# Optimization experiments

Measured on AMD Instinct MI355X. Metric: run time of the kernel, lower is better.

The kernel has to match this reference:

```python
import jax, jax.numpy as jnp
import numpy as np

N = 50000   # nodes
E = 800000  # edges per graph
FD = 128    # input feature dim (sc and fc)
H = 128     # hidden_dim
G = 64      # graphs in batch
C = 2       # num_classes


def _sage(x, src, dst, Wl, Wr, b, n):
    # PyG SAGEConv (mean aggr): lin_l(mean_{j->i} x_j) + lin_r(x_i); bias lives in lin_l.
    msum = jax.ops.segment_sum(x[src], dst, num_segments=n)          # [n, F]
    cnt = jax.ops.segment_sum(jnp.ones((src.shape[0],), x.dtype), dst, num_segments=n)
    mean = msum / jnp.maximum(cnt, 1.0)[:, None]
    return mean @ Wl.T + x @ Wr.T + b


def setup_inputs() -> dict:
    key = jax.random.key(0)
    ks = jax.random.split(key, 24)
    s = 0.05
    inp = {
        "sc_x": jax.random.normal(ks[0], (N, FD), jnp.float32),
        "fc_x": jax.random.normal(ks[1], (N, FD), jnp.float32),
        "sc_edge_index": jax.random.randint(ks[2], (2, E), 0, N),
        "fc_edge_index": jax.random.randint(ks[3], (2, E), 0, N),
        "batch": jnp.sort(jax.random.randint(ks[4], (N,), 0, G)),
        # sc convs
        "sc_Wl1": jax.random.normal(ks[5], (H, FD), jnp.float32) * s,
        "sc_Wr1": jax.random.normal(ks[6], (H, FD), jnp.float32) * s,
        "sc_b1": jnp.zeros((H,), jnp.float32),
        "sc_Wl2": jax.random.normal(ks[7], (H, H), jnp.float32) * s,
        "sc_Wr2": jax.random.normal(ks[8], (H, H), jnp.float32) * s,
        "sc_b2": jnp.zeros((H,), jnp.float32),
        # fc convs
        "fc_Wl1": jax.random.normal(ks[9], (H, FD), jnp.float32) * s,
        "fc_Wr1": jax.random.normal(ks[10], (H, FD), jnp.float32) * s,
        "fc_b1": jnp.zeros((H,), jnp.float32),
        "fc_Wl2": jax.random.normal(ks[11], (H, H), jnp.float32) * s,
        "fc_Wr2": jax.random.normal(ks[12], (H, H), jnp.float32) * s,
        "fc_b2": jnp.zeros((H,), jnp.float32),
        # MLP head
        "W1": jax.random.normal(ks[13], (H, 2 * H), jnp.float32) * s,
        "bh1": jnp.zeros((H,), jnp.float32),
        "W2": jax.random.normal(ks[14], (H // 2, H), jnp.float32) * s,
        "bh2": jnp.zeros((H // 2,), jnp.float32),
        "W3": jax.random.normal(ks[15], (C, H // 2), jnp.float32) * s,
        "bh3": jnp.zeros((C,), jnp.float32),
    }
    return inp


def reference(sc_x, fc_x, sc_edge_index, fc_edge_index, batch,
              sc_Wl1, sc_Wr1, sc_b1, sc_Wl2, sc_Wr2, sc_b2,
              fc_Wl1, fc_Wr1, fc_b1, fc_Wl2, fc_Wr2, fc_b2,
              W1, bh1, W2, bh2, W3, bh3):
    # edge_index[0] = source j, edge_index[1] = target i (PyG convention)
    sc_src, sc_dst = sc_edge_index[0], sc_edge_index[1]
    fc_src, fc_dst = fc_edge_index[0], fc_edge_index[1]

    h = jax.nn.relu(_sage(sc_x, sc_src, sc_dst, sc_Wl1, sc_Wr1, sc_b1, N))
    h = jax.nn.relu(_sage(h, sc_src, sc_dst, sc_Wl2, sc_Wr2, sc_b2, N))
    sc_pool = jax.ops.segment_sum(h, batch, num_segments=G)  # global_add_pool -> [G, H]

    g = jax.nn.relu(_sage(fc_x, fc_src, fc_dst, fc_Wl1, fc_Wr1, fc_b1, N))
    g = jax.nn.relu(_sage(g, fc_src, fc_dst, fc_Wl2, fc_Wr2, fc_b2, N))
    fc_pool = jax.ops.segment_sum(g, batch, num_segments=G)  # [G, H]

    x = jnp.concatenate([sc_pool, fc_pool], axis=1)          # [G, 2H]
    # dropout is identity in eval mode
    x = jax.nn.relu(x @ W1.T + bh1)
    x = jax.nn.relu(x @ W2.T + bh2)
    return jax.nn.log_softmax(x @ W3.T + bh3, axis=-1)       # [G, C]
```

## Files before the change

### kernel.cpp

```cpp
#include <hip/hip_runtime.h>
#include <hip/hip_bf16.h>

#define N_NODES 50000
#define E_EDGES 800000
#define G_GRAPHS 64
#define NBUCK 392
#define BCAP 5120

typedef __attribute__((ext_vector_type(8))) short s16x8;
typedef __attribute__((ext_vector_type(4))) float f32x4;

constexpr size_t O_POOL   = 0;
constexpr size_t O_GCUR   = 16384;
constexpr size_t O_BSTART = 16896;
constexpr size_t O_ROW    = 17408;
constexpr size_t O_CNT    = 117408;
constexpr size_t O_ES     = 217408;
constexpr size_t O_WB     = 1817408;
constexpr size_t O_XB     = 1882944;
constexpr size_t O_MEAN   = 5082944;
constexpr size_t O_HB     = 8282944;
constexpr size_t ZERO_BYTES = (16384 + 512) * 4;

__device__ __forceinline__ unsigned short f2bf(float f) {
    __hip_bfloat16 h = __float2bfloat16(f);
    return *reinterpret_cast<unsigned short*>(&h);
}
__device__ __forceinline__ float bflo(unsigned int v) { return __uint_as_float(v << 16); }
__device__ __forceinline__ float bfhi(unsigned int v) { return __uint_as_float(v & 0xffff0000u); }

__global__ void __launch_bounds__(512) bin_pass1(const int* __restrict__ sc_e,
                                                 const int* __restrict__ fc_e,
                                                 int* __restrict__ gcur,
                                                 unsigned int* __restrict__ buf) {
    __shared__ int hcnt[512];
    __shared__ int hexcl[512];
    __shared__ int hcur[512];
    __shared__ int gbase[512];
    __shared__ int wsum[8];
    __shared__ unsigned int stage[4096];

    const int tid = threadIdx.x;
    const int lane = tid & 63;
    const int wid = tid >> 6;
    const int tile0 = blockIdx.x * 4096;

    hcnt[tid] = 0;
    __syncthreads();

    int eb[8];
    unsigned int pk[8];
    #pragma unroll
    for (int j = 0; j < 8; ++j) {
        int ec = tile0 + j * 512 + tid;
        if (ec < 2 * E_EDGES) {
            int set = (ec >= E_EDGES);
            int local = ec - set * E_EDGES;
            const int* ep = set ? fc_e : sc_e;
            int src = ep[local];
            int dst = ep[E_EDGES + local];
            eb[j] = set * 196 + (dst >> 8);
            pk[j] = ((unsigned int)(dst & 255) << 16) | (unsigned int)src;
            atomicAdd(&hcnt[eb[j]], 1);
        } else eb[j] = -1;
    }
    __syncthreads();

    {
        int v = hcnt[tid];
        int incl = v;
        #pragma unroll
        for (int d = 1; d < 64; d <<= 1) {
            int u = __shfl_up(incl, d, 64);
            if (lane >= d) incl += u;
        }
        if (lane == 63) wsum[wid] = incl;
        __syncthreads();
        int pre = 0;
        for (int w = 0; w < wid; ++w) pre += wsum[w];
        int excl = incl - v + pre;
        hexcl[tid] = excl;
        hcur[tid] = excl;
    }
    __syncthreads();

    if (tid < NBUCK) {
        int c = hcnt[tid];
        gbase[tid] = c ? atomicAdd(&gcur[tid], c) : 0;
    }

    #pragma unroll
    for (int j = 0; j < 8; ++j) {
        if (eb[j] >= 0) {
            int pos = atomicAdd(&hcur[eb[j]], 1);
            stage[pos] = pk[j];
        }
    }
    __syncthreads();

    for (int b = wid; b < NBUCK; b += 8) {
        int c = hcnt[b];
        if (!c) continue;
        int s = hexcl[b];
        int g0 = gbase[b];
        for (int i = lane; i < c; i += 64) {
            int gi = g0 + i;
            if (gi < BCAP) buf[(size_t)b * BCAP + gi] = stage[s + i];
        }
    }
}

__global__ void bstart_scan(const int* __restrict__ gcur, int* __restrict__ bstart) {
    __shared__ int wsum[8];
    int t = threadIdx.x;
    int lane = t & 63, wid = t >> 6;
    int v = (t < NBUCK) ? min(gcur[t], BCAP) : 0;
    int incl = v;
    #pragma unroll
    for (int d = 1; d < 64; d <<= 1) {
        int u = __shfl_up(incl, d, 64);
        if (lane >= d) incl += u;
    }
    if (lane == 63) wsum[wid] = incl;
    __syncthreads();
    int pre = 0;
    for (int w = 0; w < wid; ++w) pre += wsum[w];
    if (t < NBUCK) bstart[t] = incl - v + pre;
}

__global__ void __launch_bounds__(256) bin_pass2(const unsigned int* __restrict__ buf,
                                                 const int* __restrict__ gcur,
                                                 const int* __restrict__ bstart,
                                                 int* __restrict__ row,
                                                 int* __restrict__ cnt,
                                                 int* __restrict__ es) {
    __shared__ int cntl[256];
    __shared__ int pexcl[256];
    __shared__ int pcur[256];
    __shared__ int wsum[4];
    __shared__ int stage[BCAP];

    const int b = blockIdx.x;
    const int tid = threadIdx.x;
    const int lane = tid & 63, wid = tid >> 6;
    const int sz = min(gcur[b], BCAP);
    const unsigned int* mybuf = buf + (size_t)b * BCAP;
    const int n0 = (b % 196) * 256;
    const int setbase = (b / 196) * N_NODES;

    cntl[tid] = 0;
    __syncthreads();
    for (int i = tid; i < sz; i += 256)
        atomicAdd(&cntl[mybuf[i] >> 16], 1);
    __syncthreads();
    {
        int v = cntl[tid];
        int incl = v;
        #pragma unroll
        for (int d = 1; d < 64; d <<= 1) {
            int u = __shfl_up(incl, d, 64);
            if (lane >= d) incl += u;
        }
        if (lane == 63) wsum[wid] = incl;
        __syncthreads();
        int pre = 0;
        for (int w = 0; w < wid; ++w) pre += wsum[w];
        int excl = incl - v + pre;
        pexcl[tid] = excl;
        pcur[tid] = excl;
    }
    __syncthreads();
    for (int i = tid; i < sz; i += 256) {
        unsigned int p = mybuf[i];
        int pos = atomicAdd(&pcur[p >> 16], 1);
        stage[pos] = (int)(p & 0xFFFFu);
    }
    __syncthreads();
    const int base = bstart[b];
    for (int i = tid; i < sz; i += 256) es[base + i] = stage[i];
    int node = n0 + tid;
    if (node < N_NODES) {
        cnt[setbase + node] = cntl[tid];
        row[setbase + node] = base + pexcl[tid];
    }
}

__global__ void cvt_w_kernel(const float* w0, const float* w1, const float* w2, const float* w3,
                             const float* w4, const float* w5, const float* w6, const float* w7,
                             unsigned short* __restrict__ wb) {
    const float* W;
    int m = blockIdx.y;
    switch (m) {
        case 0: W = w0; break; case 1: W = w1; break;
        case 2: W = w2; break; case 3: W = w3; break;
        case 4: W = w4; break; case 5: W = w5; break;
        case 6: W = w6; break; default: W = w7; break;
    }
    int i = blockIdx.x * 256 + threadIdx.x;
    wb[(size_t)m * 16384 + i] = f2bf(W[i]);
}

__global__ void cvt_x_kernel(const float* __restrict__ src, unsigned short* __restrict__ dst) {
    int i = blockIdx.x * 256 + threadIdx.x;
    if (i >= (N_NODES * 128) / 8) return;
    const float4* s = reinterpret_cast<const float4*>(src) + (size_t)i * 2;
    float4 a = s[0], b = s[1];
    union { s16x8 v; unsigned short u[8]; } p;
    p.u[0] = f2bf(a.x); p.u[1] = f2bf(a.y); p.u[2] = f2bf(a.z); p.u[3] = f2bf(a.w);
    p.u[4] = f2bf(b.x); p.u[5] = f2bf(b.y); p.u[6] = f2bf(b.z); p.u[7] = f2bf(b.w);
    reinterpret_cast<s16x8*>(dst)[i] = p.v;
}

__global__ void __launch_bounds__(256) agg_kernel(const unsigned short* __restrict__ x,
                                                  const int* __restrict__ row,
                                                  const int* __restrict__ cnt,
                                                  const int* __restrict__ es,
                                                  unsigned short* __restrict__ mean,
                                                  int nodebase) {
    int wave = (blockIdx.x * 256 + threadIdx.x) >> 6;
    int lane = threadIdx.x & 63;
    if (wave >= N_NODES) return;
    int gi = nodebase + wave;
    int start = row[gi];
    int deg = cnt[gi];
    float ax = 0.f, ay = 0.f;
    for (int c = 0; c < deg; c += 64) {
        int m = min(64, deg - c);
        int eid = (lane < m) ? es[start + c + lane] : 0;
        int j = 0;
        for (; j + 4 <= m; j += 4) {
            int s0 = __shfl(eid, j,     64);
            int s1 = __shfl(eid, j + 1, 64);
            int s2 = __shfl(eid, j + 2, 64);
            int s3 = __shfl(eid, j + 3, 64);
            unsigned int v0 = *reinterpret_cast<const unsigned int*>(x + (size_t)s0 * 128 + lane * 2);
            unsigned int v1 = *reinterpret_cast<const unsigned int*>(x + (size_t)s1 * 128 + lane * 2);
            unsigned int v2 = *reinterpret_cast<const unsigned int*>(x + (size_t)s2 * 128 + lane * 2);
            unsigned int v3 = *reinterpret_cast<const unsigned int*>(x + (size_t)s3 * 128 + lane * 2);
            ax += bflo(v0) + bflo(v1) + bflo(v2) + bflo(v3);
            ay += bfhi(v0) + bfhi(v1) + bfhi(v2) + bfhi(v3);
        }
        for (; j < m; ++j) {
            int s = __shfl(eid, j, 64);
            unsigned int v = *reinterpret_cast<const unsigned int*>(x + (size_t)s * 128 + lane * 2);
            ax += bflo(v); ay += bfhi(v);
        }
    }
    float inv = 1.0f / fmaxf((float)deg, 1.0f);
    unsigned int r = (unsigned int)f2bf(ax * inv) | ((unsigned int)f2bf(ay * inv) << 16);
    *reinterpret_cast<unsigned int*>(mean + (size_t)wave * 128 + lane * 2) = r;
}

__global__ void __launch_bounds__(256) gemm_mfma(const unsigned short* __restrict__ Am,
                                                 const unsigned short* __restrict__ Ax,
                                                 const unsigned short* __restrict__ Bl,
                                                 const unsigned short* __restrict__ Br,
                                                 const float* __restrict__ bias,
                                                 unsigned short* __restrict__ outH,
                                                 float* __restrict__ pool,
                                                 const int* __restrict__ batch,
                                                 int poolBase) {
    __shared__ s16x8 lds_a[2][256];
    __shared__ s16x8 lds_b[2][512];

    const int tid = threadIdx.x;
    const int lane = tid & 63;
    const int w = tid >> 6;
    const int node0 = blockIdx.x * 64;

    const int wr = w >> 1;
    const int wc = w & 1;
    const int fr = lane & 15;
    const int fg = lane >> 4;

    f32x4 acc[2][4];
    #pragma unroll
    for (int mf = 0; mf < 2; ++mf)
        #pragma unroll
        for (int nf = 0; nf < 4; ++nf) acc[mf][nf] = (f32x4){0.f, 0.f, 0.f, 0.f};

    const int sa_row = tid >> 2, sa_slot = tid & 3;
    const int sa_g = sa_slot ^ ((sa_row >> 1) & 3);
    const size_t a_off = (size_t)min(node0 + sa_row, N_NODES - 1) * 128 + sa_g * 8;
    const int sb_row0 = tid >> 2;
    const size_t b_off0 = (size_t)sb_row0 * 128 + (sa_slot ^ ((sb_row0 >> 1) & 3)) * 8;
    const int sb_row1 = 64 + (tid >> 2);
    const size_t b_off1 = (size_t)sb_row1 * 128 + (sa_slot ^ ((sb_row1 >> 1) & 3)) * 8;

    const int arow0 = wr * 32 + fr;
    const int arow1 = arow0 + 16;
    const int aidx0 = arow0 * 4 + (fg ^ ((arow0 >> 1) & 3));
    const int aidx1 = arow1 * 4 + (fg ^ ((arow1 >> 1) & 3));
    int bidx[4];
    #pragma unroll
    for (int nf = 0; nf < 4; ++nf) {
        int br = wc * 64 + nf * 16 + fr;
        bidx[nf] = br * 4 + (fg ^ ((br >> 1) & 3));
    }

    #define LOAD_A(kc) (*reinterpret_cast<const s16x8*>(((kc) < 4 ? Am : Ax) + (((kc) & 3) * 32) + a_off))
    #define LOAD_B0(kc) (*reinterpret_cast<const s16x8*>(((kc) < 4 ? Bl : Br) + (((kc) & 3) * 32) + b_off0))
    #define LOAD_B1(kc) (*reinterpret_cast<const s16x8*>(((kc) < 4 ? Bl : Br) + (((kc) & 3) * 32) + b_off1))

    {
        s16x8 ra = LOAD_A(0), rb0 = LOAD_B0(0), rb1 = LOAD_B1(0);
        lds_a[0][tid] = ra; lds_b[0][tid] = rb0; lds_b[0][256 + tid] = rb1;
    }
    __syncthreads();

    #pragma unroll
    for (int kc = 0; kc < 8; ++kc) {
        const int cur = kc & 1;
        s16x8 ra, rb0, rb1;
        if (kc < 7) { ra = LOAD_A(kc + 1); rb0 = LOAD_B0(kc + 1); rb1 = LOAD_B1(kc + 1); }
        s16x8 a0 = lds_a[cur][aidx0];
        s16x8 a1 = lds_a[cur][aidx1];
        #pragma unroll
        for (int nf = 0; nf < 4; ++nf) {
            s16x8 bv = lds_b[cur][bidx[nf]];
            acc[0][nf] = __builtin_amdgcn_mfma_f32_16x16x32_bf16(a0, bv, acc[0][nf], 0, 0, 0);
            acc[1][nf] = __builtin_amdgcn_mfma_f32_16x16x32_bf16(a1, bv, acc[1][nf], 0, 0, 0);
        }
        if (kc < 7) { lds_a[cur ^ 1][tid] = ra; lds_b[cur ^ 1][tid] = rb0; lds_b[cur ^ 1][256 + tid] = rb1; }
        __syncthreads();
    }
    #undef LOAD_A
    #undef LOAD_B0
    #undef LOAD_B1

    if (outH) {
        #pragma unroll
        for (int mf = 0; mf < 2; ++mf)
            #pragma unroll
            for (int nf = 0; nf < 4; ++nf) {
                int col = wc * 64 + nf * 16 + fr;
                float bv = bias[col];
                #pragma unroll
                for (int r = 0; r < 4; ++r) {
                    int node = node0 + wr * 32 + mf * 16 + fg * 4 + r;
                    if (node < N_NODES)
                        outH[(size_t)node * 128 + col] = f2bf(fmaxf(acc[mf][nf][r] + bv, 0.f));
                }
            }
    } else {
        int gids[2][4];
        #pragma unroll
        for (int mf = 0; mf < 2; ++mf)
            #pragma unroll
            for (int r = 0; r < 4; ++r) {
                int node = node0 + wr * 32 + mf * 16 + fg * 4 + r;
                gids[mf][r] = (node < N_NODES) ? batch[node] : -1;
            }
        #pragma unroll
        for (int nf = 0; nf < 4; ++nf) {
            int col = wc * 64 + nf * 16 + fr;
            float bv = bias[col];
            float* pbase = &pool[poolBase + col];
            int curg = -1; float s = 0.f;
            #pragma unroll
            for (int mf = 0; mf < 2; ++mf)
                #pragma unroll
                for (int r = 0; r < 4; ++r) {
                    int g = gids[mf][r];
                    if (g < 0) continue;
                    float v = fmaxf(acc[mf][nf][r] + bv, 0.f);
                    if (g != curg) {
                        if (curg >= 0) atomicAdd(pbase + (size_t)curg * 256, s);
                        curg = g; s = v;
                    } else s += v;
                }
            if (curg >= 0) atomicAdd(pbase + (size_t)curg * 256, s);
        }
    }
}

__global__ void __launch_bounds__(128) head_kernel(const float* __restrict__ pool,
                                                   const float* __restrict__ W1, const float* __restrict__ bh1,
                                                   const float* __restrict__ W2, const float* __restrict__ bh2,
                                                   const float* __restrict__ W3, const float* __restrict__ bh3,
                                                   float* __restrict__ out) {
    __shared__ float xg[256];
    __shared__ float h1[128];
    __shared__ float h2[64];
    __shared__ float lg[2];
    int g = blockIdx.x, t = threadIdx.x;
    xg[t] = pool[(size_t)g * 256 + t];
    xg[t + 128] = pool[(size_t)g * 256 + 128 + t];
    __syncthreads();
    float s = bh1[t];
    for (int k = 0; k < 256; ++k) s += W1[t * 256 + k] * xg[k];
    h1[t] = fmaxf(s, 0.f);
    __syncthreads();
    if (t < 64) {
        float s2 = bh2[t];
        for (int k = 0; k < 128; ++k) s2 += W2[t * 128 + k] * h1[k];
        h2[t] = fmaxf(s2, 0.f);
    }
    __syncthreads();
    if (t < 2) {
        float s3 = bh3[t];
        for (int k = 0; k < 64; ++k) s3 += W3[t * 64 + k] * h2[k];
        lg[t] = s3;
    }
    __syncthreads();
    if (t == 0) {
        float m = fmaxf(lg[0], lg[1]);
        float lse = m + logf(expf(lg[0] - m) + expf(lg[1] - m));
        out[g * 2 + 0] = lg[0] - lse;
        out[g * 2 + 1] = lg[1] - lse;
    }
}

extern "C" void kernel_launch(void* const* d_in, const int* in_sizes, int n_in,
                              void* d_out, int out_size, void* d_ws, size_t ws_size,
                              hipStream_t stream) {
    const float* sc_x = (const float*)d_in[0];
    const float* fc_x = (const float*)d_in[1];
    const int* sc_e   = (const int*)d_in[2];
    const int* fc_e   = (const int*)d_in[3];
    const int* batch  = (const int*)d_in[4];
    const float* sc_Wl1 = (const float*)d_in[5];
    const float* sc_Wr1 = (const float*)d_in[6];
    const float* sc_b1  = (const float*)d_in[7];
    const float* sc_Wl2 = (const float*)d_in[8];
    const float* sc_Wr2 = (const float*)d_in[9];
    const float* sc_b2  = (const float*)d_in[10];
    const float* fc_Wl1 = (const float*)d_in[11];
    const float* fc_Wr1 = (const float*)d_in[12];
    const float* fc_b1  = (const float*)d_in[13];
    const float* fc_Wl2 = (const float*)d_in[14];
    const float* fc_Wr2 = (const float*)d_in[15];
    const float* fc_b2  = (const float*)d_in[16];
    const float* W1  = (const float*)d_in[17];
    const float* bh1 = (const float*)d_in[18];
    const float* W2  = (const float*)d_in[19];
    const float* bh2 = (const float*)d_in[20];
    const float* W3  = (const float*)d_in[21];
    const float* bh3 = (const float*)d_in[22];

    int* iw = (int*)d_ws;
    float* fw = (float*)d_ws;
    float* pool = fw + O_POOL;
    int* gcur   = iw + O_GCUR;
    int* bstart = iw + O_BSTART;
    int* row    = iw + O_ROW;
    int* cnt    = iw + O_CNT;
    int* es     = iw + O_ES;
    unsigned short* WB    = (unsigned short*)(iw + O_WB);
    unsigned short* xb    = (unsigned short*)(iw + O_XB);
    unsigned short* meanb = (unsigned short*)(iw + O_MEAN);
    unsigned short* hb    = (unsigned short*)(iw + O_HB);
    unsigned int* buf = (unsigned int*)(iw + O_MEAN);

    hipMemsetAsync(d_ws, 0, ZERO_BYTES, stream);

    bin_pass1<<<(2 * E_EDGES + 4095) / 4096, 512, 0, stream>>>(sc_e, fc_e, gcur, buf);
    bstart_scan<<<1, 512, 0, stream>>>(gcur, bstart);
    bin_pass2<<<NBUCK, 256, 0, stream>>>(buf, gcur, bstart, row, cnt, es);

    cvt_w_kernel<<<dim3(64, 8), 256, 0, stream>>>(sc_Wl1, sc_Wr1, sc_Wl2, sc_Wr2,
                                                  fc_Wl1, fc_Wr1, fc_Wl2, fc_Wr2, WB);

    const int AGB = (N_NODES + 3) / 4;
    const int CVB = ((N_NODES * 128) / 8 + 255) / 256;
    const int GGB = (N_NODES + 63) / 64;

    cvt_x_kernel<<<CVB, 256, 0, stream>>>(sc_x, xb);
    agg_kernel<<<AGB, 256, 0, stream>>>(xb, row, cnt, es, meanb, 0);
    gemm_mfma<<<GGB, 256, 0, stream>>>(meanb, xb, WB + 0 * 16384, WB + 1 * 16384, sc_b1,
                                       hb, nullptr, nullptr, 0);
    agg_kernel<<<AGB, 256, 0, stream>>>(hb, row, cnt, es, meanb, 0);
    gemm_mfma<<<GGB, 256, 0, stream>>>(meanb, hb, WB + 2 * 16384, WB + 3 * 16384, sc_b2,
                                       nullptr, pool, batch, 0);
    cvt_x_kernel<<<CVB, 256, 0, stream>>>(fc_x, xb);
    agg_kernel<<<AGB, 256, 0, stream>>>(xb, row, cnt, es, meanb, N_NODES);
    gemm_mfma<<<GGB, 256, 0, stream>>>(meanb, xb, WB + 4 * 16384, WB + 5 * 16384, fc_b1,
                                       hb, nullptr, nullptr, 0);
    agg_kernel<<<AGB, 256, 0, stream>>>(hb, row, cnt, es, meanb, N_NODES);
    gemm_mfma<<<GGB, 256, 0, stream>>>(meanb, hb, WB + 6 * 16384, WB + 7 * 16384, fc_b2,
                                       nullptr, pool, batch, 128);

    head_kernel<<<G_GRAPHS, 128, 0, stream>>>(pool, W1, bh1, W2, bh2, W3, bh3, (float*)d_out);
}
```

Before: 390.8 us.

## Batch sc and fc branches into shared launches and use quarter-wave 16-byte gathers

Handles the sc and fc graphs in the same kernel launches: one conversion covers both feature sets, and the aggregation and GEMM kernels use a doubled grid, with workspace buffers resized to hold both sets. The aggregation now assigns 16 lanes per node and loads 16 bytes per lane, so a wave processes four nodes in parallel instead of issuing 4-byte loads for one node. This cuts launch count and raises memory-level parallelism and grid fill. In exchange it doubles intermediate buffer footprint, and low-degree nodes may leave quarter-waves idle.

```diff
diff --git a/kernel.cpp b/kernel.cpp
--- a/kernel.cpp
+++ b/kernel.cpp
@@ -6,6 +6,7 @@
 #define G_GRAPHS 64
 #define NBUCK 392
 #define BCAP 5120
+#define NF ((size_t)N_NODES * 128)
 
 typedef __attribute__((ext_vector_type(8))) short s16x8;
 typedef __attribute__((ext_vector_type(4))) float f32x4;
@@ -18,8 +19,8 @@
 constexpr size_t O_ES     = 217408;
 constexpr size_t O_WB     = 1817408;
 constexpr size_t O_XB     = 1882944;
-constexpr size_t O_MEAN   = 5082944;
-constexpr size_t O_HB     = 8282944;
+constexpr size_t O_MEAN   = 8282944;
+constexpr size_t O_HB     = 14682944;
 constexpr size_t ZERO_BYTES = (16384 + 512) * 4;
 
 __device__ __forceinline__ unsigned short f2bf(float f) {
@@ -200,10 +201,14 @@
     wb[(size_t)m * 16384 + i] = f2bf(W[i]);
 }
 
-__global__ void cvt_x_kernel(const float* __restrict__ src, unsigned short* __restrict__ dst) {
+__global__ void cvt_x_kernel(const float* __restrict__ sc_x, const float* __restrict__ fc_x,
+                             unsigned short* __restrict__ dst) {
     int i = blockIdx.x * 256 + threadIdx.x;
-    if (i >= (N_NODES * 128) / 8) return;
-    const float4* s = reinterpret_cast<const float4*>(src) + (size_t)i * 2;
+    if (i >= 2 * (N_NODES * 128) / 8) return;
+    int set = (i >= (N_NODES * 128) / 8);
+    int local = i - set * (N_NODES * 128) / 8;
+    const float* src = set ? fc_x : sc_x;
+    const float4* s = reinterpret_cast<const float4*>(src) + (size_t)local * 2;
     float4 a = s[0], b = s[1];
     union { s16x8 v; unsigned short u[8]; } p;
     p.u[0] = f2bf(a.x); p.u[1] = f2bf(a.y); p.u[2] = f2bf(a.z); p.u[3] = f2bf(a.w);
@@ -215,58 +220,82 @@
                                                   const int* __restrict__ row,
                                                   const int* __restrict__ cnt,
                                                   const int* __restrict__ es,
-                                                  unsigned short* __restrict__ mean,
-                                                  int nodebase) {
+                                                  unsigned short* __restrict__ mean) {
     int wave = (blockIdx.x * 256 + threadIdx.x) >> 6;
     int lane = threadIdx.x & 63;
-    if (wave >= N_NODES) return;
-    int gi = nodebase + wave;
-    int start = row[gi];
-    int deg = cnt[gi];
-    float ax = 0.f, ay = 0.f;
-    for (int c = 0; c < deg; c += 64) {
-        int m = min(64, deg - c);
-        int eid = (lane < m) ? es[start + c + lane] : 0;
+    int ql = lane & 15;
+    int n = wave * 4 + (lane >> 4);
+    if (n >= 2 * N_NODES) return;
+    const unsigned short* xs = x + (n >= N_NODES ? NF : 0);
+    int start = row[n];
+    int deg = cnt[n];
+    float a0 = 0.f, a1 = 0.f, a2 = 0.f, a3 = 0.f, a4 = 0.f, a5 = 0.f, a6 = 0.f, a7 = 0.f;
+    int qbase = lane & 48;
+    for (int c = 0; c < deg; c += 16) {
+        int m = min(16, deg - c);
+        int eid = (ql < m) ? es[start + c + ql] : 0;
         int j = 0;
         for (; j + 4 <= m; j += 4) {
-            int s0 = __shfl(eid, j,     64);
-            int s1 = __shfl(eid, j + 1, 64);
-            int s2 = __shfl(eid, j + 2, 64);
-            int s3 = __shfl(eid, j + 3, 64);
-            unsigned int v0 = *reinterpret_cast<const unsigned int*>(x + (size_t)s0 * 128 + lane * 2);
-            unsigned int v1 = *reinterpret_cast<const unsigned int*>(x + (size_t)s1 * 128 + lane * 2);
-            unsigned int v2 = *reinterpret_cast<const unsigned int*>(x + (size_t)s2 * 128 + lane * 2);
-            unsigned int v3 = *reinterpret_cast<const unsigned int*>(x + (size_t)s3 * 128 + lane * 2);
-            ax += bflo(v0) + bflo(v1) + bflo(v2) + bflo(v3);
-            ay += bfhi(v0) + bfhi(v1) + bfhi(v2) + bfhi(v3);
+            int s0 = __shfl(eid, qbase + j,     64);
+            int s1 = __shfl(eid, qbase + j + 1, 64);
+            int s2 = __shfl(eid, qbase + j + 2, 64);
+            int s3 = __shfl(eid, qbase + j + 3, 64);
+            uint4 v0 = *reinterpret_cast<const uint4*>(xs + (size_t)s0 * 128 + ql * 8);
+            uint4 v1 = *reinterpret_cast<const uint4*>(xs + (size_t)s1 * 128 + ql * 8);
+            uint4 v2 = *reinterpret_cast<const uint4*>(xs + (size_t)s2 * 128 + ql * 8);
+            uint4 v3 = *reinterpret_cast<const uint4*>(xs + (size_t)s3 * 128 + ql * 8);
+            a0 += bflo(v0.x) + bflo(v1.x) + bflo(v2.x) + bflo(v3.x);
+            a1 += bfhi(v0.x) + bfhi(v1.x) + bfhi(v2.x) + bfhi(v3.x);
+            a2 += bflo(v0.y) + bflo(v1.y) + bflo(v2.y) + bflo(v3.y);
+            a3 += bfhi(v0.y) + bfhi(v1.y) + bfhi(v2.y) + bfhi(v3.y);
+            a4 += bflo(v0.z) + bflo(v1.z) + bflo(v2.z) + bflo(v3.z);
+            a5 += bfhi(v0.z) + bfhi(v1.z) + bfhi(v2.z) + bfhi(v3.z);
+            a6 += bflo(v0.w) + bflo(v1.w) + bflo(v2.w) + bflo(v3.w);
+            a7 += bfhi(v0.w) + bfhi(v1.w) + bfhi(v2.w) + bfhi(v3.w);
         }
         for (; j < m; ++j) {
-            int s = __shfl(eid, j, 64);
-            unsigned int v = *reinterpret_cast<const unsigned int*>(x + (size_t)s * 128 + lane * 2);
-            ax += bflo(v); ay += bfhi(v);
+            int s = __shfl(eid, qbase + j, 64);
+            uint4 v = *reinterpret_cast<const uint4*>(xs + (size_t)s * 128 + ql * 8);
+            a0 += bflo(v.x); a1 += bfhi(v.x);
+            a2 += bflo(v.y); a3 += bfhi(v.y);
+            a4 += bflo(v.z); a5 += bfhi(v.z);
+            a6 += bflo(v.w); a7 += bfhi(v.w);
         }
     }
     float inv = 1.0f / fmaxf((float)deg, 1.0f);
-    unsigned int r = (unsigned int)f2bf(ax * inv) | ((unsigned int)f2bf(ay * inv) << 16);
-    *reinterpret_cast<unsigned int*>(mean + (size_t)wave * 128 + lane * 2) = r;
-}
-
-__global__ void __launch_bounds__(256) gemm_mfma(const unsigned short* __restrict__ Am,
-                                                 const unsigned short* __restrict__ Ax,
-                                                 const unsigned short* __restrict__ Bl,
-                                                 const unsigned short* __restrict__ Br,
-                                                 const float* __restrict__ bias,
-                                                 unsigned short* __restrict__ outH,
+    uint4 o;
+    o.x = (unsigned int)f2bf(a0 * inv) | ((unsigned int)f2bf(a1 * inv) << 16);
+    o.y = (unsigned int)f2bf(a2 * inv) | ((unsigned int)f2bf(a3 * inv) << 16);
+    o.z = (unsigned int)f2bf(a4 * inv) | ((unsigned int)f2bf(a5 * inv) << 16);
+    o.w = (unsigned int)f2bf(a6 * inv) | ((unsigned int)f2bf(a7 * inv) << 16);
+    *reinterpret_cast<uint4*>(mean + (size_t)n * 128 + ql * 8) = o;
+}
+
+__global__ void __launch_bounds__(256) gemm_mfma(const unsigned short* __restrict__ AmB,
+                                                 const unsigned short* __restrict__ AxB,
+                                                 const unsigned short* __restrict__ WBall,
+                                                 const float* __restrict__ bias0,
+                                                 const float* __restrict__ bias1,
+                                                 unsigned short* __restrict__ outHB,
                                                  float* __restrict__ pool,
                                                  const int* __restrict__ batch,
-                                                 int poolBase) {
+                                                 int layer) {
     __shared__ s16x8 lds_a[2][256];
     __shared__ s16x8 lds_b[2][512];
 
     const int tid = threadIdx.x;
     const int lane = tid & 63;
     const int w = tid >> 6;
+    const int set = blockIdx.y;
     const int node0 = blockIdx.x * 64;
+
+    const unsigned short* Am = AmB + (size_t)set * NF;
+    const unsigned short* Ax = AxB + (size_t)set * NF;
+    const unsigned short* Bl = WBall + (size_t)(set * 4 + layer * 2) * 16384;
+    const unsigned short* Br = Bl + 16384;
+    const float* bias = set ? bias1 : bias0;
+    unsigned short* outH = outHB ? outHB + (size_t)set * NF : nullptr;
+    const int poolBase = set * 128;
 
     const int wr = w >> 1;
     const int wc = w & 1;
@@ -460,25 +489,15 @@
 
     cvt_w_kernel<<<dim3(64, 8), 256, 0, stream>>>(sc_Wl1, sc_Wr1, sc_Wl2, sc_Wr2,
                                                   fc_Wl1, fc_Wr1, fc_Wl2, fc_Wr2, WB);
-
-    const int AGB = (N_NODES + 3) / 4;
-    const int CVB = ((N_NODES * 128) / 8 + 255) / 256;
-    const int GGB = (N_NODES + 63) / 64;
-
-    cvt_x_kernel<<<CVB, 256, 0, stream>>>(sc_x, xb);
-    agg_kernel<<<AGB, 256, 0, stream>>>(xb, row, cnt, es, meanb, 0);
-    gemm_mfma<<<GGB, 256, 0, stream>>>(meanb, xb, WB + 0 * 16384, WB + 1 * 16384, sc_b1,
-                                       hb, nullptr, nullptr, 0);
-    agg_kernel<<<AGB, 256, 0, stream>>>(hb, row, cnt, es, meanb, 0);
-    gemm_mfma<<<GGB, 256, 0, stream>>>(meanb, hb, WB + 2 * 16384, WB + 3 * 16384, sc_b2,
-                                       nullptr, pool, batch, 0);
-    cvt_x_kernel<<<CVB, 256, 0, stream>>>(fc_x, xb);
-    agg_kernel<<<AGB, 256, 0, stream>>>(xb, row, cnt, es, meanb, N_NODES);
-    gemm_mfma<<<GGB, 256, 0, stream>>>(meanb, xb, WB + 4 * 16384, WB + 5 * 16384, fc_b1,
-                                       hb, nullptr, nullptr, 0);
-    agg_kernel<<<AGB, 256, 0, stream>>>(hb, row, cnt, es, meanb, N_NODES);
-    gemm_mfma<<<GGB, 256, 0, stream>>>(meanb, hb, WB + 6 * 16384, WB + 7 * 16384, fc_b2,
-                                       nullptr, pool, batch, 128);
+    cvt_x_kernel<<<2 * 3125, 256, 0, stream>>>(sc_x, fc_x, xb);
+
+    const int AGB = (2 * N_NODES + 15) / 16;
+    dim3 gg((N_NODES + 63) / 64, 2);
+
+    agg_kernel<<<AGB, 256, 0, stream>>>(xb, row, cnt, es, meanb);
+    gemm_mfma<<<gg, 256, 0, stream>>>(meanb, xb, WB, sc_b1, fc_b1, hb, nullptr, nullptr, 0);
+    agg_kernel<<<AGB, 256, 0, stream>>>(hb, row, cnt, es, meanb);
+    gemm_mfma<<<gg, 256, 0, stream>>>(meanb, hb, WB, sc_b2, fc_b2, nullptr, pool, batch, 1);
 
     head_kernel<<<G_GRAPHS, 128, 0, stream>>>(pool, W1, bh1, W2, bh2, W3, bh3, (float*)d_out);
 }
```

New measurement: 351.5 us. 10.1% less time.
